# Kernel tuning notes

Hardware: AMD Instinct MI355X
Metric: run time of the kernel (lower is better)

Reference implementation:

```python
import jax, jax.numpy as jnp
import numpy as np

B, T, H, HY, E, L = 32, 256, 1024, 256, 64, 2


def setup_inputs() -> dict:
    key = jax.random.key(0)
    ks = jax.random.split(key, 16)
    rn = lambda k, s, sc=0.05: jax.random.normal(k, s, dtype=jnp.float32) * sc
    return {
        'input': rn(ks[0], (B, T, H), 1.0),
        'w_ih': rn(ks[1], (L, 4 * H, H)),
        'w_hh': rn(ks[2], (L, 4 * H, H)),
        'hyper_w_ih': rn(ks[3], (L, 4 * HY, 2 * H)),
        'hyper_w_hh': rn(ks[4], (L, 4 * HY, HY)),
        'hyper_b': rn(ks[5], (L, 4 * HY)),
        'w_zh': rn(ks[6], (L, 4 * E, HY)),
        'b_zh': jnp.ones((L, 4 * E), jnp.float32),
        'w_zx': rn(ks[7], (L, 4 * E, HY)),
        'b_zx': jnp.ones((L, 4 * E), jnp.float32),
        'w_zb': rn(ks[8], (L, 4 * E, HY)),
        'w_dh': rn(ks[9], (L, 4, H, E), 1.0 / E),
        'w_dx': rn(ks[10], (L, 4, H, E), 1.0 / E),
        'w_db': rn(ks[11], (L, 4, H, E)),
        'b0': rn(ks[12], (L, 4 * H)),
    }


def reference(input, w_ih, w_hh, hyper_w_ih, hyper_w_hh, hyper_b,
              w_zh, b_zh, w_zx, b_zx, w_zb, w_dh, w_dx, w_db, b0):
    L = w_ih.shape[0]
    Bb = input.shape[0]
    Hh = w_hh.shape[-1]
    Hy = hyper_w_hh.shape[-1]
    Ee = w_dh.shape[-1]

    def cell(l, xt, h, c, hh, hc):
        # hyper (meta) LSTM step: input is concat(x, h_main)
        xh = jnp.concatenate([xt, h], axis=-1)
        hg = xh @ hyper_w_ih[l].T + hh @ hyper_w_hh[l].T + hyper_b[l]
        hi, hf, hgc, ho = jnp.split(hg, 4, axis=-1)
        hc2 = jax.nn.sigmoid(hf) * hc + jax.nn.sigmoid(hi) * jnp.tanh(hgc)
        hh2 = jax.nn.sigmoid(ho) * jnp.tanh(hc2)
        # gate-wise embeddings z (B, 4, E) then project to per-gate scale vectors (B, 4H)
        zh = (hh2 @ w_zh[l].T + b_zh[l]).reshape(Bb, 4, Ee)
        zx = (hh2 @ w_zx[l].T + b_zx[l]).reshape(Bb, 4, Ee)
        zb = (hh2 @ w_zb[l].T).reshape(Bb, 4, Ee)
        dh = jnp.einsum('bge,ghe->bgh', zh, w_dh[l]).reshape(Bb, 4 * Hh)
        dx = jnp.einsum('bge,ghe->bgh', zx, w_dx[l]).reshape(Bb, 4 * Hh)
        db = jnp.einsum('bge,ghe->bgh', zb, w_db[l]).reshape(Bb, 4 * Hh) + b0[l]
        # main LSTM gates, dynamically scaled by hypernetwork
        pre = dh * (h @ w_hh[l].T) + dx * (xt @ w_ih[l].T) + db
        i, f, g, o = jnp.split(pre, 4, axis=-1)
        c2 = jax.nn.sigmoid(f) * c + jax.nn.sigmoid(i) * jnp.tanh(g)
        h2 = jax.nn.sigmoid(o) * jnp.tanh(c2)
        return h2, c2, hh2, hc2

    def step(carry, xt):
        h, c, hh, hc = carry  # each (L, B, .)
        hs, cs, hhs, hcs = [], [], [], []
        inp = xt
        for l in range(L):
            h2, c2, hh2, hc2 = cell(l, inp, h[l], c[l], hh[l], hc[l])
            inp = h2
            hs.append(h2); cs.append(c2); hhs.append(hh2); hcs.append(hc2)
        carry = (jnp.stack(hs), jnp.stack(cs), jnp.stack(hhs), jnp.stack(hcs))
        return carry, inp  # top-layer hidden

    init = (jnp.zeros((L, Bb, Hh), input.dtype), jnp.zeros((L, Bb, Hh), input.dtype),
            jnp.zeros((L, Bb, Hy), input.dtype), jnp.zeros((L, Bb, Hy), input.dtype))
    carry, ys = jax.lax.scan(step, init, jnp.swapaxes(input, 0, 1))
    h_seq = jnp.swapaxes(ys, 0, 1)  # (B, T, H)
    return h_seq, carry[0][-1], carry[1][-1]
```

## Files before the change

### kernel.cpp

```cpp
#include <hip/hip_runtime.h>

typedef __bf16 bf16;
typedef __bf16 bf16x8 __attribute__((ext_vector_type(8)));
typedef __bf16 bf16x4 __attribute__((ext_vector_type(4)));
typedef float f32x4 __attribute__((ext_vector_type(4)));
typedef unsigned long long u64;

#define SCOPE_AGENT __HIP_MEMORY_SCOPE_AGENT


__device__ __forceinline__ float sigf(float x) { return 1.0f / (1.0f + __expf(-x)); }
__device__ __forceinline__ float tanhf_fast(float x) {
  float e = __expf(-2.0f * fabsf(x));
  float r = (1.0f - e) / (1.0f + e);
  return copysignf(r, x);
}
__device__ __forceinline__ f32x4 mfma16(bf16x8 a, bf16x8 b, f32x4 c) {
  return __builtin_amdgcn_mfma_f32_16x16x32_bf16(a, b, c, 0, 0, 0);
}
__device__ __forceinline__ u64 uld(const u64* p) { return __hip_atomic_load(p, __ATOMIC_RELAXED, SCOPE_AGENT); }
__device__ __forceinline__ void ust(u64* p, u64 v) { __hip_atomic_store(p, v, __ATOMIC_RELAXED, SCOPE_AGENT); }
__device__ __forceinline__ int ildi(const int* p) { return __hip_atomic_load(p, __ATOMIC_RELAXED, SCOPE_AGENT); }
__device__ __forceinline__ void isti(int* p, int v) { __hip_atomic_store(p, v, __ATOMIC_RELAXED, SCOPE_AGENT); }
__device__ __forceinline__ void fstf(float* p, float v) { __hip_atomic_store(p, v, __ATOMIC_RELAXED, SCOPE_AGENT); }

__global__ void detect_kernel(const void* probe, int* flag) {
  __shared__ int cnt;
  if (threadIdx.x == 0) cnt = 0;
  __syncthreads();
  const bf16* p = (const bf16*)probe;
  int local = 0;
  for (int j = threadIdx.x; j < 8192; j += 256) {
    float x = (float)p[j];
    bool wild = (x != x) || (fabsf(x) > 1e3f) || (x != 0.0f && fabsf(x) < 1e-30f);
    local += wild ? 1 : 0;
  }
  atomicAdd(&cnt, local);
  __syncthreads();
  if (threadIdx.x == 0) *flag = (cnt > 64) ? 1 : 0;
}

struct CvtSrc { const void* s[15]; };
struct CvtDst { bf16* d[15]; };

__global__ __launch_bounds__(256) void convert_kernel(CvtSrc S, CvtDst D, const int* flag) {
  const int pre[16] = {0, 8388608, 16777216, 25165824, 29360128, 29884416, 29886464,
                       30017536, 30018048, 30149120, 30149632, 30280704, 30804992,
                       31329280, 31853568, 31861760};
  const int fp32 = *flag;
  const int nvec = 31861760 / 4;
  for (int v = blockIdx.x * 256 + threadIdx.x; v < nvec; v += gridDim.x * 256) {
    int e = v * 4;
    int seg = 0;
#pragma unroll
    for (int k = 1; k < 15; ++k) seg += (e >= pre[k]) ? 1 : 0;
    int off = e - pre[seg];
    bf16* d = D.d[seg] + off;
    if (fp32) {
      const float* s = (const float*)S.s[seg] + off;
      float4 x = *(const float4*)s;
      d[0] = (bf16)x.x; d[1] = (bf16)x.y; d[2] = (bf16)x.z; d[3] = (bf16)x.w;
    } else {
      const bf16* s = (const bf16*)S.s[seg] + off;
      d[0] = s[0]; d[1] = s[1]; d[2] = s[2]; d[3] = s[3];
    }
  }
}

__global__ void init_kernel(u64* zbase) {
  int i = blockIdx.x * 256 + threadIdx.x;
  zbase[i] = 0ull;
}

__global__ __launch_bounds__(256) void gemm_pre(
    const bf16* __restrict__ A, const bf16* __restrict__ w_ih_l,
    const bf16* __restrict__ hwih_l, bf16* __restrict__ Xp, float* __restrict__ Hxp) {
  constexpr int LDT = 72;
  __shared__ alignas(16) bf16 As[64 * LDT];
  __shared__ alignas(16) bf16 Bs[64 * LDT];
  const int bm = blockIdx.x & 127;
  const int bn = blockIdx.x >> 7;
  const int m0 = bm * 64, n0 = bn * 64;
  const int tid = threadIdx.x;
  const int lane = tid & 63, wid = tid >> 6;
  const int l15 = lane & 15, q = lane >> 4;
  const int srow = tid >> 2, sk = (tid & 3) * 16;
  const bf16* arow = A + (size_t)(m0 + srow) * 1024;
  const int n = n0 + srow;
  const bf16* brow = (n < 4096) ? (w_ih_l + (size_t)n * 1024)
                                : (hwih_l + (size_t)(n - 4096) * 2048);
  f32x4 acc[4] = {};
  for (int kb = 0; kb < 1024; kb += 64) {
    *(bf16x8*)(&As[srow * LDT + sk])     = *(const bf16x8*)(arow + kb + sk);
    *(bf16x8*)(&As[srow * LDT + sk + 8]) = *(const bf16x8*)(arow + kb + sk + 8);
    *(bf16x8*)(&Bs[srow * LDT + sk])     = *(const bf16x8*)(brow + kb + sk);
    *(bf16x8*)(&Bs[srow * LDT + sk + 8]) = *(const bf16x8*)(brow + kb + sk + 8);
    __syncthreads();
#pragma unroll
    for (int kk = 0; kk < 64; kk += 32) {
      bf16x8 av = *(const bf16x8*)(&As[(wid * 16 + l15) * LDT + kk + q * 8]);
#pragma unroll
      for (int j = 0; j < 4; ++j) {
        bf16x8 bv = *(const bf16x8*)(&Bs[(j * 16 + l15) * LDT + kk + q * 8]);
        acc[j] = mfma16(av, bv, acc[j]);
      }
    }
    __syncthreads();
  }
#pragma unroll
  for (int j = 0; j < 4; ++j) {
    const int gn = n0 + j * 16 + l15;
#pragma unroll
    for (int r = 0; r < 4; ++r) {
      const int gm = m0 + wid * 16 + q * 4 + r;
      float v = acc[j][r];
      if (gn < 4096) Xp[(size_t)gm * 4096 + gn] = (bf16)v;
      else           Hxp[(size_t)gm * 1024 + (gn - 4096)] = v;
    }
  }
}

struct SeqArgs {
  const bf16 *w_hh, *hwih, *hwhh, *hyb;
  const bf16 *w_zh, *b_zh, *w_zx, *b_zx, *w_zb;
  const bf16 *w_dh, *w_dx, *w_db, *b0;
  const bf16 *Xp; const float *Hxp;
  const bf16 *w_ih1;
  bf16 *Xp1c; float *Hxp1c;
  u64 *Y0;
  u64 *hpub, *hhpub; float *hgpub;
  float *outp;
  int *flags;
};

__global__ __launch_bounds__(256) void seq_kernel(SeqArgs a) {
  __shared__ char smem[60160] __attribute__((aligned(16)));
  bf16 (*hstage)[520]  = (bf16(*)[520])smem;
  bf16 (*hhstage)[264] = (bf16(*)[264])(smem + 33280);
  bf16 (*hA4)[1032]   = (bf16(*)[1032])smem;
  bf16 (*hh2A)[264]   = (bf16(*)[264])(smem + 16512);
  float (*RhL)[256]   = (float(*)[256])(smem + 18624);
  float (*hgs)[1024]  = (float(*)[1024])(smem + 26816);
  float (*zsL)[768]   = (float(*)[768])(smem + 43200);
  float (*presL)[256] = (float(*)[256])(smem + 55488);
  bf16 (*hbuf)[64]    = (bf16(*)[64])(smem + 59584);
  bf16*  As = (bf16*)smem;
  bf16*  Bs = (bf16*)(smem + 9216);
  float* Ct = (float*)(smem + 18432);

  const int tid = threadIdx.x;
  const int lane = tid & 63, wid = tid >> 6;
  const int l15 = lane & 15, q = lane >> 4;
  const int blk = blockIdx.x;
  const int xcd = blk & 7, slot = blk >> 3;
  const int layer = xcd >> 2, xl = xcd & 3;
  const int s16 = xl * 4 + (slot & 3);
  const int bq = slot >> 2;
  const int lblk = bq * 16 + s16;
  const bool isHyper = ((s16 >> 1) == bq);
  const int hj = bq * 2 + (s16 & 1);

  u64*   hpub  = a.hpub  + layer * 8192;
  u64*   hhpub = a.hhpub + layer * 2048;
  float* hgpub = a.hgpub + layer * 32768;
  int* genp0  = a.flags;
  int* genp   = a.flags + layer * 16;
  int* gchunkp= a.flags + 32;
  int* arrp   = a.flags + 64 + layer * 2048;
  int* hgfp   = a.flags + 4160 + layer * 256;
  int* carrp  = a.flags + 4672;

  const bf16* whh_l = a.w_hh + (size_t)layer * 4194304;
  const bf16* hybl  = a.hyb + layer * 1024;
  const bf16* bzh_l = a.b_zh + layer * 256;
  const bf16* bzx_l = a.b_zx + layer * 256;
  const bf16* b0_l  = a.b0 + (size_t)layer * 4096;
  const int cb = tid >> 6, chl = tid & 63;

  float c_reg = 0.0f;
  float hc[4] = {0,0,0,0};

  const bf16* zrow[12];
#pragma unroll
  for (int j = 0; j < 12; ++j) {
    int ng = wid * 12 + j, tau = ng >> 4;
    const bf16* base = (tau == 0) ? a.w_zh : (tau == 1) ? a.w_zx : a.w_zb;
    zrow[j] = base + ((size_t)layer * 256 + (ng & 15) * 16 + l15) * 256;
  }
  const bf16* rrow[4];
#pragma unroll
  for (int nt = 0; nt < 4; ++nt)
    rrow[nt] = whh_l + (size_t)(wid * 1024 + s16 * 64 + nt * 16 + l15) * 1024;
  const size_t wdo = ((size_t)(layer * 4 + wid) * 1024 + s16 * 64 + lane) * 64;
  const bf16 *pdh = a.w_dh + wdo, *pdx = a.w_dx + wdo, *pdb = a.w_db + wdo;

  for (int t = 0; t < 256; ++t) {
    const int tloc = t & 31;

    if (layer == 1 && tloc == 0) {
      const int k = t >> 5;
      if (tid == 0) { while (ildi(genp0) < (k + 1) * 32) __builtin_amdgcn_s_sleep(2); }
      __atomic_signal_fence(__ATOMIC_SEQ_CST);
      __syncthreads();
      const int srow = tid >> 2, sk = (tid & 3) * 16;
      for (int tt = 0; tt < 10; ++tt) {
        const int tile = lblk * 10 + tt;
        const int m0 = (tile & 15) * 64, n0 = (tile >> 4) * 64;
        const int m = m0 + srow;
        const u64* arow = a.Y0 + (((size_t)(m >> 5) * 256 + k * 32 + (m & 31)) << 8);
        const int n = n0 + srow;
        const bf16* brow = (n < 4096) ? (a.w_ih1 + (size_t)n * 1024)
                                      : (a.hwih + 2097152 + (size_t)(n - 4096) * 2048);
        f32x4 acc[4] = {};
        for (int kb = 0; kb < 1024; kb += 64) {
          const int c0 = (kb + sk) >> 2;
          u64 a0 = uld(arow + c0),     a1 = uld(arow + c0 + 1);
          u64 a2 = uld(arow + c0 + 2), a3 = uld(arow + c0 + 3);
          *(u64*)&As[srow * 72 + sk]      = a0;
          *(u64*)&As[srow * 72 + sk + 4]  = a1;
          *(u64*)&As[srow * 72 + sk + 8]  = a2;
          *(u64*)&As[srow * 72 + sk + 12] = a3;
          *(bf16x8*)&Bs[srow * 72 + sk]     = *(const bf16x8*)(brow + kb + sk);
          *(bf16x8*)&Bs[srow * 72 + sk + 8] = *(const bf16x8*)(brow + kb + sk + 8);
          __syncthreads();
#pragma unroll
          for (int kk = 0; kk < 64; kk += 32) {
            bf16x8 av = *(const bf16x8*)&As[(wid * 16 + l15) * 72 + kk + q * 8];
#pragma unroll
            for (int j = 0; j < 4; ++j) {
              bf16x8 bv = *(const bf16x8*)&Bs[(j * 16 + l15) * 72 + kk + q * 8];
              acc[j] = mfma16(av, bv, acc[j]);
            }
          }
          __syncthreads();
        }
#pragma unroll
        for (int j = 0; j < 4; ++j)
#pragma unroll
          for (int r = 0; r < 4; ++r)
            Ct[(wid * 16 + q * 4 + r) * 64 + j * 16 + l15] = acc[j][r];
        __syncthreads();
#pragma unroll
        for (int e = 0; e < 4; ++e) {
          const int qd = tid * 4 + e;
          const int row = qd >> 4, col4 = (qd & 15) * 4;
          f32x4 v = *(const f32x4*)&Ct[row * 64 + col4];
          const int gm = m0 + row, gn = n0 + col4;
          if (gn < 4096) {
            union { bf16 h[4]; u64 u; } pk;
#pragma unroll
            for (int x = 0; x < 4; ++x) pk.h[x] = (bf16)v[x];
            ust((u64*)a.Xp1c + ((((size_t)gm << 12) + gn) >> 2), pk.u);
          } else {
            float* hp = a.Hxp1c + ((size_t)gm << 10) + (gn - 4096);
#pragma unroll
            for (int x = 0; x < 4; ++x) fstf(hp + x, v[x]);
          }
        }
        __syncthreads();
      }
      __atomic_signal_fence(__ATOMIC_SEQ_CST);
      __builtin_amdgcn_s_waitcnt(0);
      __syncthreads();
      if (tid == 0) isti(carrp + lblk * 16, k + 1);
      if (lblk == 0 && wid == 0) {
        for (;;) {
          int v0 = ildi(carrp + lane * 32);
          int v1 = ildi(carrp + lane * 32 + 16);
          if (__all((v0 >= k + 1) && (v1 >= k + 1))) break;
          __builtin_amdgcn_s_sleep(2);
        }
        __atomic_signal_fence(__ATOMIC_SEQ_CST);
        if (lane == 0) isti(gchunkp, k + 1);
      }
      if (tid == 0) { while (ildi(gchunkp) < k + 1) __builtin_amdgcn_s_sleep(2); }
      __atomic_signal_fence(__ATOMIC_SEQ_CST);
      __syncthreads();
    }

    if (t > 0 && tid == 0) {
      while (ildi(genp) < t) __builtin_amdgcn_s_sleep(2);
    }
    __atomic_signal_fence(__ATOMIC_SEQ_CST);
    __syncthreads();

    if (isHyper) {
      for (int i = tid; i < 2048; i += 256) {
        int b = i >> 6, u = i & 63;
        *(u64*)&hhstage[b][u * 4] = uld(hhpub + i);
      }
      for (int i = tid; i < 4096; i += 256) {
        int b = i >> 7, u = i & 127;
        *(u64*)&hstage[b][u * 4] = uld(hpub + ((size_t)b << 8) + u);
      }
      __syncthreads();
      const bf16* bih = a.hwih + (size_t)layer * 2097152
                        + (size_t)(hj * 64 + wid * 16 + l15) * 2048 + 1024;
      f32x4 cA = {}, cB = {};
      for (int kk = 0; kk < 512; kk += 32) {
        int ko = kk + q * 8;
        bf16x8 bv = *(const bf16x8*)(bih + ko);
        bf16x8 a0 = *(const bf16x8*)&hstage[l15][ko];
        bf16x8 a1 = *(const bf16x8*)&hstage[16 + l15][ko];
        cA = mfma16(a0, bv, cA); cB = mfma16(a1, bv, cB);
      }
      __syncthreads();
      for (int i = tid; i < 4096; i += 256) {
        int b = i >> 7, u = i & 127;
        *(u64*)&hstage[b][u * 4] = uld(hpub + ((size_t)b << 8) + 128 + u);
      }
      __syncthreads();
      for (int kk = 0; kk < 512; kk += 32) {
        int ko = kk + q * 8;
        bf16x8 bv = *(const bf16x8*)(bih + 512 + ko);
        bf16x8 a0 = *(const bf16x8*)&hstage[l15][ko];
        bf16x8 a1 = *(const bf16x8*)&hstage[16 + l15][ko];
        cA = mfma16(a0, bv, cA); cB = mfma16(a1, bv, cB);
      }
      const bf16* bhh = a.hwhh + (size_t)layer * 262144
                      + (size_t)(hj * 64 + wid * 16 + l15) * 256;
      for (int kk = 0; kk < 256; kk += 32) {
        int ko = kk + q * 8;
        bf16x8 bv = *(const bf16x8*)(bhh + ko);
        bf16x8 a0 = *(const bf16x8*)&hhstage[l15][ko];
        bf16x8 a1 = *(const bf16x8*)&hhstage[16 + l15][ko];
        cA = mfma16(a0, bv, cA); cB = mfma16(a1, bv, cB);
      }
      const int n = hj * 64 + wid * 16 + l15;
#pragma unroll
      for (int r = 0; r < 4; ++r) {
        fstf(hgpub + (q * 4 + r) * 1024 + n, cA[r]);
        fstf(hgpub + (16 + q * 4 + r) * 1024 + n, cB[r]);
      }
      __atomic_signal_fence(__ATOMIC_SEQ_CST);
      __builtin_amdgcn_s_waitcnt(0);
      __syncthreads();
      if (tid == 0) isti(hgfp + hj * 16, t + 1);
    }
    __syncthreads();

    for (int i = tid; i < 1024; i += 256) {
      int b = i >> 8, u = i & 255;
      *(u64*)&hA4[b][u * 4] = uld(hpub + ((size_t)(bq * 4 + b) << 8) + u);
    }
    __syncthreads();
    {
      f32x4 racc[4] = {};
      for (int kk = 0; kk < 1024; kk += 32) {
        const int ko = kk + q * 8;
        bf16x8 av = *(const bf16x8*)&hA4[l15 & 3][ko];
#pragma unroll
        for (int nt = 0; nt < 4; ++nt) {
          bf16x8 bv = *(const bf16x8*)(rrow[nt] + ko);
          racc[nt] = mfma16(av, bv, racc[nt]);
        }
      }
      if (lane < 16) {
#pragma unroll
        for (int nt = 0; nt < 4; ++nt)
#pragma unroll
          for (int r = 0; r < 4; ++r)
            RhL[r][wid * 64 + nt * 16 + lane] = racc[nt][r];
      }
    }
    if (tid < 16) { while (ildi(hgfp + tid * 16) < t + 1) __builtin_amdgcn_s_sleep(1); }
    __atomic_signal_fence(__ATOMIC_SEQ_CST);
    __syncthreads();
    {
      const u64* hg64 = (const u64*)hgpub + ((size_t)bq << 11);
      for (int i = tid; i < 2048; i += 256) {
        int b = i >> 9, u = i & 511;
        *(u64*)&hgs[b][u * 2] = uld(hg64 + ((size_t)b << 9) + u);
      }
    }
    __syncthreads();
    {
      const float* hgr = hgs[cb];
      const int d0 = chl * 4;
      float hxv[4][4];
      if (layer == 0) {
        const float* hxr = a.Hxp + ((size_t)(bq * 4 + cb) * 256 + t) * 1024;
#pragma unroll
        for (int g = 0; g < 4; ++g)
#pragma unroll
          for (int dd = 0; dd < 4; ++dd) hxv[g][dd] = hxr[g * 256 + d0 + dd];
      } else {
        const u64* hxr = (const u64*)a.Hxp1c
                       + ((size_t)((bq * 4 + cb) * 32 + tloc) << 9);
#pragma unroll
        for (int g = 0; g < 4; ++g) {
          u64 w0 = uld(hxr + g * 128 + chl * 2);
          u64 w1 = uld(hxr + g * 128 + chl * 2 + 1);
          hxv[g][0] = __uint_as_float((unsigned)(w0 & 0xffffffffu));
          hxv[g][1] = __uint_as_float((unsigned)(w0 >> 32));
          hxv[g][2] = __uint_as_float((unsigned)(w1 & 0xffffffffu));
          hxv[g][3] = __uint_as_float((unsigned)(w1 >> 32));
        }
      }
      float hh2v[4];
#pragma unroll
      for (int dd = 0; dd < 4; ++dd) {
        int d = d0 + dd;
        float hi  = hgr[d]       + (float)hybl[d]       + hxv[0][dd];
        float hf  = hgr[256 + d] + (float)hybl[256 + d] + hxv[1][dd];
        float hgv = hgr[512 + d] + (float)hybl[512 + d] + hxv[2][dd];
        float ho  = hgr[768 + d] + (float)hybl[768 + d] + hxv[3][dd];
        hc[dd] = sigf(hf) * hc[dd] + sigf(hi) * tanhf_fast(hgv);
        float v = sigf(ho) * tanhf_fast(hc[dd]);
        hh2v[dd] = v;
        hh2A[cb][d] = (bf16)v;
      }
      if (s16 == 0) {
        union { bf16 h[4]; u64 v; } pk;
#pragma unroll
        for (int dd = 0; dd < 4; ++dd) pk.h[dd] = (bf16)hh2v[dd];
        ust(hhpub + ((size_t)(bq * 4 + cb) << 6) + chl, pk.v);
      }
    }
    __syncthreads();
    {
      f32x4 zacc[12] = {};
      for (int kk = 0; kk < 256; kk += 32) {
        const int ko = kk + q * 8;
        bf16x8 av = *(const bf16x8*)&hh2A[l15 & 3][ko];
#pragma unroll
        for (int j = 0; j < 12; ++j) {
          bf16x8 bv = *(const bf16x8*)(zrow[j] + ko);
          zacc[j] = mfma16(av, bv, zacc[j]);
        }
      }
      if (lane < 16) {
#pragma unroll
        for (int j = 0; j < 12; ++j) {
          int ng = wid * 12 + j, tau = ng >> 4, col = (ng & 15) * 16 + lane;
          float bias = (tau == 0) ? (float)bzh_l[col] : (tau == 1) ? (float)bzx_l[col] : 0.0f;
#pragma unroll
          for (int r = 0; r < 4; ++r) zsL[r][tau * 256 + col] = zacc[j][r] + bias;
        }
      }
    }
    __syncthreads();
    {
      float dH[4] = {}, dX[4] = {}, dB[4] = {};
      for (int e0 = 0; e0 < 64; e0 += 4) {
        bf16x4 wh = *(const bf16x4*)(pdh + e0);
        bf16x4 wx = *(const bf16x4*)(pdx + e0);
        bf16x4 wb = *(const bf16x4*)(pdb + e0);
        f32x4 zh_[4], zx_[4], zb_[4];
#pragma unroll
        for (int b = 0; b < 4; ++b) {
          zh_[b] = *(const f32x4*)&zsL[b][wid * 64 + e0];
          zx_[b] = *(const f32x4*)&zsL[b][256 + wid * 64 + e0];
          zb_[b] = *(const f32x4*)&zsL[b][512 + wid * 64 + e0];
        }
#pragma unroll
        for (int jj = 0; jj < 4; ++jj) {
          float whf = (float)wh[jj], wxf = (float)wx[jj], wbf = (float)wb[jj];
#pragma unroll
          for (int b = 0; b < 4; ++b) {
            dH[b] += zh_[b][jj] * whf;
            dX[b] += zx_[b][jj] * wxf;
            dB[b] += zb_[b][jj] * wbf;
          }
        }
      }
      const int n = wid * 1024 + s16 * 64 + lane;
#pragma unroll
      for (int b = 0; b < 4; ++b) {
        float rh = RhL[b][wid * 64 + lane];
        float xp;
        if (layer == 0) {
          xp = (float)a.Xp[((size_t)(bq * 4 + b) * 256 + t) * 4096 + n];
        } else {
          u64 w = uld((const u64*)a.Xp1c
                      + ((((size_t)((bq * 4 + b) * 32 + tloc) << 12) + (n & ~3)) >> 2));
          xp = __uint_as_float(((unsigned)(w >> ((n & 3) * 16)) & 0xffffu) << 16);
        }
        float b0v = (float)b0_l[n];
        presL[b][wid * 64 + lane] = dH[b] * rh + dX[b] * xp + dB[b] + b0v;
      }
    }
    __syncthreads();
    {
      float iv = presL[cb][chl];
      float fv = presL[cb][64 + chl];
      float gv = presL[cb][128 + chl];
      float ov = presL[cb][192 + chl];
      c_reg = sigf(fv) * c_reg + sigf(iv) * tanhf_fast(gv);
      float hn = sigf(ov) * tanhf_fast(c_reg);
      hbuf[cb][chl] = (bf16)hn;
      if (layer) {
        const size_t oo = ((size_t)(bq * 4 + cb) * 256 + t) * 1024 + s16 * 64 + chl;
        a.outp[oo] = hn;
        if (t == 255) {
          a.outp[8388608 + (bq * 4 + cb) * 1024 + s16 * 64 + chl] = hn;
          a.outp[8421376 + (bq * 4 + cb) * 1024 + s16 * 64 + chl] = c_reg;
        }
      }
    }
    __syncthreads();
    if (tid < 64) {
      int b = tid >> 4, u = tid & 15;
      u64 pk = *(const u64*)&hbuf[b][u * 4];
      ust(hpub + ((size_t)(bq * 4 + b) << 8) + s16 * 16 + u, pk);
      if (layer == 0)
        ust(a.Y0 + (((size_t)(bq * 4 + b) * 256 + t) << 8) + s16 * 16 + u, pk);
    }
    __atomic_signal_fence(__ATOMIC_SEQ_CST);
    __builtin_amdgcn_s_waitcnt(0);
    __syncthreads();
    if (tid == 0) isti(arrp + lblk * 16, t + 1);
    if (lblk == 0 && wid == 0) {
      const int t1 = t + 1;
      for (;;) {
        int v0 = ildi(arrp + lane * 32);
        int v1 = ildi(arrp + lane * 32 + 16);
        if (__all((v0 >= t1) && (v1 >= t1))) break;
        __builtin_amdgcn_s_sleep(2);
      }
      __atomic_signal_fence(__ATOMIC_SEQ_CST);
      if (lane == 0) isti(genp, t1);
    }
  }
}

extern "C" void kernel_launch(void* const* d_in, const int* in_sizes, int n_in,
                              void* d_out, int out_size, void* d_ws, size_t ws_size,
                              hipStream_t stream) {
  float* outp = (float*)d_out;
  char* ws = (char*)d_ws;
  bf16*  Xp     = (bf16*) (ws);
  float* Hxp    = (float*)(ws + 67108864ull);
  u64*   Y0     = (u64*)  (ws + 100663296ull);
  bf16* c_input = (bf16*)(ws + 117669888ull);
  bf16*  Xp1c   = c_input;
  float* Hxp1c  = (float*)(ws + 117669888ull + 8388608ull);
  bf16* c_w_ih  = (bf16*)(ws + 134447104ull);
  bf16* c_w_hh  = (bf16*)(ws + 151224320ull);
  bf16* c_hwih  = (bf16*)(ws + 168001536ull);
  bf16* c_hwhh  = (bf16*)(ws + 176390144ull);
  bf16* c_hyb   = (bf16*)(ws + 177438720ull);
  bf16* c_wzh   = (bf16*)(ws + 177442816ull);
  bf16* c_bzh   = (bf16*)(ws + 177704960ull);
  bf16* c_wzx   = (bf16*)(ws + 177705984ull);
  bf16* c_bzx   = (bf16*)(ws + 177968128ull);
  bf16* c_wzb   = (bf16*)(ws + 177969152ull);
  bf16* c_wdh   = (bf16*)(ws + 178231296ull);
  bf16* c_wdx   = (bf16*)(ws + 179279872ull);
  bf16* c_wdb   = (bf16*)(ws + 180328448ull);
  bf16* c_b0    = (bf16*)(ws + 181377024ull);
  int*  dflag   = (int*) (ws + 181393408ull);
  char* pubb    = ws + 181397504ull;
  u64*   hpub   = (u64*)  (pubb + 0);
  u64*   hhpub  = (u64*)  (pubb + 131072);
  float* hgpub  = (float*)(pubb + 163840);
  int*   flags  = (int*)  (pubb + 425984);

  hipLaunchKernelGGL(detect_kernel, dim3(1), dim3(256), 0, stream, d_in[2], dflag);
  CvtSrc S; CvtDst D;
  for (int i = 0; i < 15; ++i) S.s[i] = d_in[i];
  D.d[0] = c_input; D.d[1] = c_w_ih; D.d[2] = c_w_hh; D.d[3] = c_hwih; D.d[4] = c_hwhh;
  D.d[5] = c_hyb;   D.d[6] = c_wzh;  D.d[7] = c_bzh;  D.d[8] = c_wzx;  D.d[9] = c_bzx;
  D.d[10] = c_wzb;  D.d[11] = c_wdh; D.d[12] = c_wdx; D.d[13] = c_wdb; D.d[14] = c_b0;
  hipLaunchKernelGGL(convert_kernel, dim3(2048), dim3(256), 0, stream, S, D, dflag);

  hipLaunchKernelGGL(init_kernel, dim3(224), dim3(256), 0, stream, (u64*)pubb);
  hipLaunchKernelGGL(gemm_pre, dim3(10240), dim3(256), 0, stream,
                     c_input, c_w_ih, c_hwih, Xp, Hxp);

  SeqArgs sa;
  sa.w_hh = c_w_hh; sa.hwih = c_hwih; sa.hwhh = c_hwhh; sa.hyb = c_hyb;
  sa.w_zh = c_wzh; sa.b_zh = c_bzh; sa.w_zx = c_wzx; sa.b_zx = c_bzx; sa.w_zb = c_wzb;
  sa.w_dh = c_wdh; sa.w_dx = c_wdx; sa.w_db = c_wdb; sa.b0 = c_b0;
  sa.Xp = Xp; sa.Hxp = Hxp;
  sa.w_ih1 = c_w_ih + (size_t)4194304;
  sa.Xp1c = Xp1c; sa.Hxp1c = Hxp1c;
  sa.Y0 = Y0;
  sa.hpub = hpub; sa.hhpub = hhpub; sa.hgpub = hgpub;
  sa.outp = outp;
  sa.flags = flags;
  hipLaunchKernelGGL(seq_kernel, dim3(256), dim3(256), 0, stream, sa);
}
```

Measured before the change: 22.79 ms.

## Fuse hyper-LSTM cell into hyper blocks and double-buffer hidden-state publication

```diff
diff --git a/kernel.cpp b/kernel.cpp
--- a/kernel.cpp
+++ b/kernel.cpp
@@ -23,6 +23,7 @@
 __device__ __forceinline__ int ildi(const int* p) { return __hip_atomic_load(p, __ATOMIC_RELAXED, SCOPE_AGENT); }
 __device__ __forceinline__ void isti(int* p, int v) { __hip_atomic_store(p, v, __ATOMIC_RELAXED, SCOPE_AGENT); }
 __device__ __forceinline__ void fstf(float* p, float v) { __hip_atomic_store(p, v, __ATOMIC_RELAXED, SCOPE_AGENT); }
+__device__ __forceinline__ void usti32(unsigned* p, unsigned v) { __hip_atomic_store(p, v, __ATOMIC_RELAXED, SCOPE_AGENT); }
 
 __global__ void detect_kernel(const void* probe, int* flag) {
   __shared__ int cnt;
@@ -128,22 +129,23 @@
   const bf16 *w_ih1;
   bf16 *Xp1c; float *Hxp1c;
   u64 *Y0;
-  u64 *hpub, *hhpub; float *hgpub;
+  u64 *hpub;
+  u64 *hh2pub;
   float *outp;
   int *flags;
 };
 
 __global__ __launch_bounds__(256) void seq_kernel(SeqArgs a) {
-  __shared__ char smem[60160] __attribute__((aligned(16)));
-  bf16 (*hstage)[520]  = (bf16(*)[520])smem;
-  bf16 (*hhstage)[264] = (bf16(*)[264])(smem + 33280);
+  __shared__ char smem[41472] __attribute__((aligned(16)));
+  bf16 (*hstage)[1032] = (bf16(*)[1032])smem;
+  bf16 (*hhK)[264]    = (bf16(*)[264])(smem + 33024);
+  float* hgL          = (float*)(smem + 33024);
   bf16 (*hA4)[1032]   = (bf16(*)[1032])smem;
-  bf16 (*hh2A)[264]   = (bf16(*)[264])(smem + 16512);
-  float (*RhL)[256]   = (float(*)[256])(smem + 18624);
-  float (*hgs)[1024]  = (float(*)[1024])(smem + 26816);
-  float (*zsL)[768]   = (float(*)[768])(smem + 43200);
-  float (*presL)[256] = (float(*)[256])(smem + 55488);
-  bf16 (*hbuf)[64]    = (bf16(*)[64])(smem + 59584);
+  bf16 (*hh2A)[264]   = (bf16(*)[264])(smem + 8256);
+  float (*RhL)[256]   = (float(*)[256])(smem + 10368);
+  float (*zsL)[768]   = (float(*)[768])(smem + 14464);
+  float (*presL)[256] = (float(*)[256])(smem + 26752);
+  bf16 (*hbuf)[64]    = (bf16(*)[64])(smem + 30848);
   bf16*  As = (bf16*)smem;
   bf16*  Bs = (bf16*)(smem + 9216);
   float* Ct = (float*)(smem + 18432);
@@ -157,17 +159,17 @@
   const int s16 = xl * 4 + (slot & 3);
   const int bq = slot >> 2;
   const int lblk = bq * 16 + s16;
-  const bool isHyper = ((s16 >> 1) == bq);
-  const int hj = bq * 2 + (s16 & 1);
-
-  u64*   hpub  = a.hpub  + layer * 8192;
-  u64*   hhpub = a.hhpub + layer * 2048;
-  float* hgpub = a.hgpub + layer * 32768;
+  const int hd = s16 >> 1;
+  const int mh = (bq == hd) ? 0 : ((bq == ((hd + 4) & 7)) ? 1 : -1);
+  const bool isHyper = (((s16 & 1) == 0) && (mh >= 0));
+
+  u64* hbase  = a.hpub + (size_t)layer * 16384;
+  u64* h2base = a.hh2pub + (size_t)layer * 4096;
   int* genp0  = a.flags;
   int* genp   = a.flags + layer * 16;
   int* gchunkp= a.flags + 32;
   int* arrp   = a.flags + 64 + layer * 2048;
-  int* hgfp   = a.flags + 4160 + layer * 256;
+  int* hh2fp  = a.flags + 4160 + layer * 256;
   int* carrp  = a.flags + 4672;
 
   const bf16* whh_l = a.w_hh + (size_t)layer * 4194304;
@@ -178,7 +180,7 @@
   const int cb = tid >> 6, chl = tid & 63;
 
   float c_reg = 0.0f;
-  float hc[4] = {0,0,0,0};
+  float hc[2] = {0, 0};
 
   const bf16* zrow[12];
 #pragma unroll
@@ -191,11 +193,23 @@
 #pragma unroll
   for (int nt = 0; nt < 4; ++nt)
     rrow[nt] = whh_l + (size_t)(wid * 1024 + s16 * 64 + nt * 16 + l15) * 1024;
+  const bf16* hirow[2];
+  const bf16* hhrow[2];
+#pragma unroll
+  for (int nt = 0; nt < 2; ++nt) {
+    const int row = wid * 256 + hd * 32 + nt * 16 + l15;
+    hirow[nt] = a.hwih + (size_t)layer * 2097152 + (size_t)row * 2048 + 1024;
+    hhrow[nt] = a.hwhh + (size_t)layer * 262144 + (size_t)row * 256;
+  }
   const size_t wdo = ((size_t)(layer * 4 + wid) * 1024 + s16 * 64 + lane) * 64;
   const bf16 *pdh = a.w_dh + wdo, *pdx = a.w_dx + wdo, *pdb = a.w_db + wdo;
 
   for (int t = 0; t < 256; ++t) {
     const int tloc = t & 31;
+    u64* wslot = hbase + (size_t)(t & 1) * 8192;
+    const u64* rslot = hbase + (size_t)((t + 1) & 1) * 8192;
+    u64* wcur = h2base + (size_t)(t & 1) * 2048;
+    const u64* rK = h2base + (size_t)((t + 1) & 1) * 2048;
 
     if (layer == 1 && tloc == 0) {
       const int k = t >> 5;
@@ -285,63 +299,84 @@
     __syncthreads();
 
     if (isHyper) {
-      for (int i = tid; i < 2048; i += 256) {
+      for (int i = tid; i < 4096; i += 256) {
+        int b = i >> 8, u = i & 255;
+        *(u64*)&hstage[b][u * 4] = uld(rslot + ((size_t)(mh * 16 + b) << 8) + u);
+      }
+      for (int i = tid; i < 1024; i += 256) {
         int b = i >> 6, u = i & 63;
-        *(u64*)&hhstage[b][u * 4] = uld(hhpub + i);
-      }
-      for (int i = tid; i < 4096; i += 256) {
-        int b = i >> 7, u = i & 127;
-        *(u64*)&hstage[b][u * 4] = uld(hpub + ((size_t)b << 8) + u);
-      }
-      __syncthreads();
-      const bf16* bih = a.hwih + (size_t)layer * 2097152
-                        + (size_t)(hj * 64 + wid * 16 + l15) * 2048 + 1024;
-      f32x4 cA = {}, cB = {};
-      for (int kk = 0; kk < 512; kk += 32) {
+        *(u64*)&hhK[b][u * 4] = uld(rK + ((size_t)(mh * 16 + b) << 6) + u);
+      }
+      __syncthreads();
+      f32x4 acc[2] = {};
+      for (int kk = 0; kk < 1024; kk += 32) {
         int ko = kk + q * 8;
-        bf16x8 bv = *(const bf16x8*)(bih + ko);
         bf16x8 a0 = *(const bf16x8*)&hstage[l15][ko];
-        bf16x8 a1 = *(const bf16x8*)&hstage[16 + l15][ko];
-        cA = mfma16(a0, bv, cA); cB = mfma16(a1, bv, cB);
-      }
-      __syncthreads();
-      for (int i = tid; i < 4096; i += 256) {
-        int b = i >> 7, u = i & 127;
-        *(u64*)&hstage[b][u * 4] = uld(hpub + ((size_t)b << 8) + 128 + u);
-      }
-      __syncthreads();
-      for (int kk = 0; kk < 512; kk += 32) {
-        int ko = kk + q * 8;
-        bf16x8 bv = *(const bf16x8*)(bih + 512 + ko);
-        bf16x8 a0 = *(const bf16x8*)&hstage[l15][ko];
-        bf16x8 a1 = *(const bf16x8*)&hstage[16 + l15][ko];
-        cA = mfma16(a0, bv, cA); cB = mfma16(a1, bv, cB);
-      }
-      const bf16* bhh = a.hwhh + (size_t)layer * 262144
-                      + (size_t)(hj * 64 + wid * 16 + l15) * 256;
+#pragma unroll
+        for (int nt = 0; nt < 2; ++nt) {
+          bf16x8 bv = *(const bf16x8*)(hirow[nt] + ko);
+          acc[nt] = mfma16(a0, bv, acc[nt]);
+        }
+      }
       for (int kk = 0; kk < 256; kk += 32) {
         int ko = kk + q * 8;
-        bf16x8 bv = *(const bf16x8*)(bhh + ko);
-        bf16x8 a0 = *(const bf16x8*)&hhstage[l15][ko];
-        bf16x8 a1 = *(const bf16x8*)&hhstage[16 + l15][ko];
-        cA = mfma16(a0, bv, cA); cB = mfma16(a1, bv, cB);
-      }
-      const int n = hj * 64 + wid * 16 + l15;
-#pragma unroll
-      for (int r = 0; r < 4; ++r) {
-        fstf(hgpub + (q * 4 + r) * 1024 + n, cA[r]);
-        fstf(hgpub + (16 + q * 4 + r) * 1024 + n, cB[r]);
+        bf16x8 a0 = *(const bf16x8*)&hhK[l15][ko];
+#pragma unroll
+        for (int nt = 0; nt < 2; ++nt) {
+          bf16x8 bv = *(const bf16x8*)(hhrow[nt] + ko);
+          acc[nt] = mfma16(a0, bv, acc[nt]);
+        }
+      }
+      __syncthreads();
+#pragma unroll
+      for (int nt = 0; nt < 2; ++nt)
+#pragma unroll
+        for (int r = 0; r < 4; ++r)
+          hgL[(wid * 16 + q * 4 + r) * 32 + nt * 16 + l15] = acc[nt][r];
+      __syncthreads();
+      {
+        const int b16 = tid >> 4, d0 = (tid & 15) * 2;
+        const int b = mh * 16 + b16;
+        float hx2[4][2];
+        if (layer == 0) {
+          const float* hx = a.Hxp + ((size_t)b * 256 + t) * 1024 + hd * 32 + d0;
+#pragma unroll
+          for (int g = 0; g < 4; ++g) {
+            hx2[g][0] = hx[g * 256]; hx2[g][1] = hx[g * 256 + 1];
+          }
+        } else {
+          const u64* hx1 = (const u64*)a.Hxp1c + (((size_t)b * 32 + tloc) << 9)
+                         + ((hd * 32 + d0) >> 1);
+#pragma unroll
+          for (int g = 0; g < 4; ++g) {
+            u64 w = uld(hx1 + g * 128);
+            hx2[g][0] = __uint_as_float((unsigned)(w & 0xffffffffu));
+            hx2[g][1] = __uint_as_float((unsigned)(w >> 32));
+          }
+        }
+        union { bf16 h[2]; unsigned u; } pk;
+#pragma unroll
+        for (int dd = 0; dd < 2; ++dd) {
+          int d = d0 + dd, gd = hd * 32 + d;
+          float hi  = hgL[(0 * 16 + b16) * 32 + d] + (float)hybl[gd]       + hx2[0][dd];
+          float hf  = hgL[(1 * 16 + b16) * 32 + d] + (float)hybl[256 + gd] + hx2[1][dd];
+          float hgv = hgL[(2 * 16 + b16) * 32 + d] + (float)hybl[512 + gd] + hx2[2][dd];
+          float ho  = hgL[(3 * 16 + b16) * 32 + d] + (float)hybl[768 + gd] + hx2[3][dd];
+          hc[dd] = sigf(hf) * hc[dd] + sigf(hi) * tanhf_fast(hgv);
+          pk.h[dd] = (bf16)(sigf(ho) * tanhf_fast(hc[dd]));
+        }
+        usti32((unsigned*)wcur + b * 128 + hd * 16 + (d0 >> 1), pk.u);
       }
       __atomic_signal_fence(__ATOMIC_SEQ_CST);
       __builtin_amdgcn_s_waitcnt(0);
       __syncthreads();
-      if (tid == 0) isti(hgfp + hj * 16, t + 1);
+      if (tid == 0) isti(hh2fp + (hd * 2 + mh) * 16, t + 1);
     }
     __syncthreads();
 
     for (int i = tid; i < 1024; i += 256) {
       int b = i >> 8, u = i & 255;
-      *(u64*)&hA4[b][u * 4] = uld(hpub + ((size_t)(bq * 4 + b) << 8) + u);
+      *(u64*)&hA4[b][u * 4] = uld(rslot + ((size_t)(bq * 4 + b) << 8) + u);
     }
     __syncthreads();
     {
@@ -363,59 +398,12 @@
             RhL[r][wid * 64 + nt * 16 + lane] = racc[nt][r];
       }
     }
-    if (tid < 16) { while (ildi(hgfp + tid * 16) < t + 1) __builtin_amdgcn_s_sleep(1); }
+    if (tid < 16) { while (ildi(hh2fp + tid * 16) < t + 1) __builtin_amdgcn_s_sleep(1); }
     __atomic_signal_fence(__ATOMIC_SEQ_CST);
     __syncthreads();
     {
-      const u64* hg64 = (const u64*)hgpub + ((size_t)bq << 11);
-      for (int i = tid; i < 2048; i += 256) {
-        int b = i >> 9, u = i & 511;
-        *(u64*)&hgs[b][u * 2] = uld(hg64 + ((size_t)b << 9) + u);
-      }
-    }
-    __syncthreads();
-    {
-      const float* hgr = hgs[cb];
-      const int d0 = chl * 4;
-      float hxv[4][4];
-      if (layer == 0) {
-        const float* hxr = a.Hxp + ((size_t)(bq * 4 + cb) * 256 + t) * 1024;
-#pragma unroll
-        for (int g = 0; g < 4; ++g)
-#pragma unroll
-          for (int dd = 0; dd < 4; ++dd) hxv[g][dd] = hxr[g * 256 + d0 + dd];
-      } else {
-        const u64* hxr = (const u64*)a.Hxp1c
-                       + ((size_t)((bq * 4 + cb) * 32 + tloc) << 9);
-#pragma unroll
-        for (int g = 0; g < 4; ++g) {
-          u64 w0 = uld(hxr + g * 128 + chl * 2);
-          u64 w1 = uld(hxr + g * 128 + chl * 2 + 1);
-          hxv[g][0] = __uint_as_float((unsigned)(w0 & 0xffffffffu));
-          hxv[g][1] = __uint_as_float((unsigned)(w0 >> 32));
-          hxv[g][2] = __uint_as_float((unsigned)(w1 & 0xffffffffu));
-          hxv[g][3] = __uint_as_float((unsigned)(w1 >> 32));
-        }
-      }
-      float hh2v[4];
-#pragma unroll
-      for (int dd = 0; dd < 4; ++dd) {
-        int d = d0 + dd;
-        float hi  = hgr[d]       + (float)hybl[d]       + hxv[0][dd];
-        float hf  = hgr[256 + d] + (float)hybl[256 + d] + hxv[1][dd];
-        float hgv = hgr[512 + d] + (float)hybl[512 + d] + hxv[2][dd];
-        float ho  = hgr[768 + d] + (float)hybl[768 + d] + hxv[3][dd];
-        hc[dd] = sigf(hf) * hc[dd] + sigf(hi) * tanhf_fast(hgv);
-        float v = sigf(ho) * tanhf_fast(hc[dd]);
-        hh2v[dd] = v;
-        hh2A[cb][d] = (bf16)v;
-      }
-      if (s16 == 0) {
-        union { bf16 h[4]; u64 v; } pk;
-#pragma unroll
-        for (int dd = 0; dd < 4; ++dd) pk.h[dd] = (bf16)hh2v[dd];
-        ust(hhpub + ((size_t)(bq * 4 + cb) << 6) + chl, pk.v);
-      }
+      int b = tid >> 6, u = tid & 63;
+      *(u64*)&hh2A[b][u * 4] = uld(wcur + ((size_t)(bq * 4 + b) << 6) + u);
     }
     __syncthreads();
     {
@@ -502,7 +490,7 @@
     if (tid < 64) {
       int b = tid >> 4, u = tid & 15;
       u64 pk = *(const u64*)&hbuf[b][u * 4];
-      ust(hpub + ((size_t)(bq * 4 + b) << 8) + s16 * 16 + u, pk);
+      ust(wslot + ((size_t)(bq * 4 + b) << 8) + s16 * 16 + u, pk);
       if (layer == 0)
         ust(a.Y0 + (((size_t)(bq * 4 + b) * 256 + t) << 8) + s16 * 16 + u, pk);
     }
@@ -552,9 +540,8 @@
   int*  dflag   = (int*) (ws + 181393408ull);
   char* pubb    = ws + 181397504ull;
   u64*   hpub   = (u64*)  (pubb + 0);
-  u64*   hhpub  = (u64*)  (pubb + 131072);
-  float* hgpub  = (float*)(pubb + 163840);
-  int*   flags  = (int*)  (pubb + 425984);
+  u64*   hh2pub = (u64*)  (pubb + 262144);
+  int*   flags  = (int*)  (pubb + 327680);
 
   hipLaunchKernelGGL(detect_kernel, dim3(1), dim3(256), 0, stream, d_in[2], dflag);
   CvtSrc S; CvtDst D;
@@ -564,7 +551,7 @@
   D.d[10] = c_wzb;  D.d[11] = c_wdh; D.d[12] = c_wdx; D.d[13] = c_wdb; D.d[14] = c_b0;
   hipLaunchKernelGGL(convert_kernel, dim3(2048), dim3(256), 0, stream, S, D, dflag);
 
-  hipLaunchKernelGGL(init_kernel, dim3(224), dim3(256), 0, stream, (u64*)pubb);
+  hipLaunchKernelGGL(init_kernel, dim3(176), dim3(256), 0, stream, (u64*)pubb);
   hipLaunchKernelGGL(gemm_pre, dim3(10240), dim3(256), 0, stream,
                      c_input, c_w_ih, c_hwih, Xp, Hxp);
 
@@ -576,7 +563,7 @@
   sa.w_ih1 = c_w_ih + (size_t)4194304;
   sa.Xp1c = Xp1c; sa.Hxp1c = Hxp1c;
   sa.Y0 = Y0;
-  sa.hpub = hpub; sa.hhpub = hhpub; sa.hgpub = hgpub;
+  sa.hpub = hpub; sa.hh2pub = hh2pub;
   sa.outp = outp;
   sa.flags = flags;
   hipLaunchKernelGGL(seq_kernel, dim3(256), dim3(256), 0, stream, sa);
```

Result: faster. 19.70 ms, median of 2 (-13.6%).
